# Kernel tuning notes

Measured on AMD Instinct MI355X. Metric: run time of the kernel, lower is better.

## Reference

```python
import jax, jax.numpy as jnp
import numpy as np

N_NODES = 100000
N_EDGES = 3200000
N_GRAPHS = 64
NEG_SLOPE = 0.2


def mish(x):
    return x * jnp.tanh(jax.nn.softplus(x))


def gat_layer(x, src, dst, W, b, a_src, a_dst, heads, out_ch, n_nodes):
    # h: [N, H, C]
    h = (x @ W).reshape(n_nodes, heads, out_ch)
    alpha_s = jnp.sum(h * a_src[None], axis=-1)  # [N, H]
    alpha_d = jnp.sum(h * a_dst[None], axis=-1)  # [N, H]
    e = jax.nn.leaky_relu(alpha_s[src] + alpha_d[dst], NEG_SLOPE)  # [E, H]
    # scatter-softmax over incoming edges of each destination node
    emax = jax.ops.segment_max(e, dst, num_segments=n_nodes)  # [N, H]
    ee = jnp.exp(e - emax[dst])
    den = jax.ops.segment_sum(ee, dst, num_segments=n_nodes)
    alpha = ee / (den[dst] + 1e-16)  # [E, H]
    msg = h[src] * alpha[..., None]  # [E, H, C]
    out = jax.ops.segment_sum(msg, dst, num_segments=n_nodes)
    return out.reshape(n_nodes, heads * out_ch) + b


def setup_inputs() -> dict:
    key = jax.random.key(0)
    ks = jax.random.split(key, 10)
    x = jax.random.normal(ks[0], (N_NODES, 128), dtype=jnp.float32)
    edge_index = jax.random.randint(ks[1], (2, N_EDGES), 0, N_NODES, dtype=jnp.int64)
    batch = jnp.sort(jax.random.randint(ks[2], (N_NODES,), 0, N_GRAPHS, dtype=jnp.int64))
    s1 = 1.0 / np.sqrt(128.0)
    s2 = 1.0 / np.sqrt(16.0)
    return {
        "x": x,
        "edge_index": edge_index,
        "batch": batch,
        "W1": jax.random.normal(ks[3], (128, 16), dtype=jnp.float32) * s1,
        "b1": jnp.zeros((16,), dtype=jnp.float32),
        "a_src1": jax.random.normal(ks[4], (4, 4), dtype=jnp.float32) * 0.5,
        "a_dst1": jax.random.normal(ks[5], (4, 4), dtype=jnp.float32) * 0.5,
        "W2": jax.random.normal(ks[6], (16, 32), dtype=jnp.float32) * s2,
        "b2": jnp.zeros((32,), dtype=jnp.float32),
        "a_src2": jax.random.normal(ks[7], (1, 32), dtype=jnp.float32) * 0.5,
        "a_dst2": jax.random.normal(ks[8], (1, 32), dtype=jnp.float32) * 0.5,
    }


def reference(x, edge_index, batch, W1, b1, a_src1, a_dst1, W2, b2, a_src2, a_dst2):
    n = x.shape[0]
    # PyG GATConv default add_self_loops=True
    loop = jnp.arange(n, dtype=edge_index.dtype)
    src = jnp.concatenate([edge_index[0], loop])
    dst = jnp.concatenate([edge_index[1], loop])
    h = mish(gat_layer(x, src, dst, W1, b1, a_src1, a_dst1, heads=4, out_ch=4, n_nodes=n))
    h = mish(gat_layer(h, src, dst, W2, b2, a_src2, a_dst2, heads=1, out_ch=32, n_nodes=n))
    # global_mean_pool
    sums = jax.ops.segment_sum(h, batch, num_segments=N_GRAPHS)
    cnts = jax.ops.segment_sum(jnp.ones((n,), h.dtype), batch, num_segments=N_GRAPHS)
    return sums / jnp.maximum(cnts, 1.0)[:, None]
```

## Files before the change

kernel.cpp:

```cpp
#include <hip/hip_runtime.h>
#include <hip/hip_fp16.h>
#include <math.h>

#define NEG_SLOPE 0.2f
#define SB 256
#define NBMAX 1024
#define CAP 5120
#define CAPH 2816

typedef _Float16 half2v __attribute__((ext_vector_type(2)));
typedef _Float16 half4v __attribute__((ext_vector_type(4)));

__device__ __forceinline__ float mishf(float x) {
    if (x > 15.f) return x;
    float ex = __expf(x);
    float y = 1.f + ex;
    float y2 = y * y;
    return x * (y2 - 1.f) / (y2 + 1.f);
}

__device__ __forceinline__ float lw(float e) {
    return __expf(fmaxf(e, NEG_SLOPE * e));
}

__device__ __forceinline__ float hdot2a(half2v a, half2v b, float c) {
#if __has_builtin(__builtin_amdgcn_fdot2)
    return __builtin_amdgcn_fdot2(a, b, c, false);
#else
    return (float)a.x * (float)b.x + (float)a.y * (float)b.y + c;
#endif
}

__global__ void gemm1_kernel(const float* __restrict__ x, const float* __restrict__ W1,
                             const float* __restrict__ a_dst,
                             const float* __restrict__ W2, const float* __restrict__ as2,
                             const float* __restrict__ ad2,
                             _Float16* __restrict__ hpre1h, float* __restrict__ addst,
                             int* __restrict__ cursor, float* __restrict__ pool,
                             float* __restrict__ cnt, float* __restrict__ vs,
                             float* __restrict__ vd, int NB, int NG, int N) {
    __shared__ float Wlt[16 * 132];
    __shared__ float xs[16 * 132];
    int tid = threadIdx.x;
    if (blockIdx.x == 0) {
        for (int i = tid; i < NB; i += 256) cursor[i] = 0;
        for (int i = tid; i < NG * 32; i += 256) pool[i] = 0.f;
        for (int i = tid; i < NG; i += 256) cnt[i] = 0.f;
        if (tid < 16) {
            float ps = 0.f, pd = 0.f;
            #pragma unroll
            for (int c = 0; c < 32; c++) {
                float w = W2[tid * 32 + c];
                ps += w * as2[c];
                pd += w * ad2[c];
            }
            vs[tid] = ps; vd[tid] = pd;
        }
    }
    for (int i = tid; i < 2048; i += 256) Wlt[(i & 15) * 132 + (i >> 4)] = W1[i];
    int nodebase = blockIdx.x * 16;
    const float4* x4 = (const float4*)(x + (size_t)nodebase * 128);
    for (int i = tid; i < 512; i += 256) {
        float4 v = x4[i];
        int e = i * 4;
        int nl = e >> 7, k = e & 127;
        float* dp = &xs[nl * 132 + k];
        dp[0] = v.x; dp[1] = v.y; dp[2] = v.z; dp[3] = v.w;
    }
    __syncthreads();
    int nl = tid >> 4, ch = tid & 15;
    const float4* xr4 = (const float4*)&xs[nl * 132];
    const float4* wr4 = (const float4*)&Wlt[ch * 132];
    float acc = 0.f;
    #pragma unroll
    for (int k4 = 0; k4 < 32; k4++) {
        float4 xv = xr4[k4];
        float4 wv = wr4[k4];
        acc += xv.x * wv.x + xv.y * wv.y + xv.z * wv.z + xv.w * wv.w;
    }
    int node = nodebase + nl;
    if (node < N) {
        hpre1h[node * 16 + ch] = (_Float16)acc;
        float pd = acc * a_dst[ch];
        pd += __shfl_xor(pd, 1); pd += __shfl_xor(pd, 2);
        if ((ch & 3) == 0) addst[node * 4 + (ch >> 2)] = pd;
    }
}

__global__ __launch_bounds__(1024) void scatF_kernel(
        const int* __restrict__ src, const int* __restrict__ dst,
        int E, int Etot, int CH, int NB,
        int* __restrict__ cursor, int* __restrict__ pairs) {
    __shared__ int lcnt[NBMAX];
    __shared__ int lbase[NBMAX];
    int tid = threadIdx.x, blk = blockIdx.x;
    for (int b = tid; b < NB; b += 1024) lcnt[b] = 0;
    __syncthreads();
    int ibeg = blk * CH, iend = min((blk + 1) * CH, Etot);
    int cd[16];
    #pragma unroll
    for (int u = 0; u < 16; u++) {
        int i = ibeg + tid + (u << 10);
        int d = -1;
        if (i < iend) d = (i < E) ? dst[i] : (i - E);
        cd[u] = d;
        if (d >= 0) atomicAdd(&lcnt[d >> 7], 1);
    }
    for (int i = ibeg + (16 << 10) + tid; i < iend; i += 1024) {
        int d = (i < E) ? dst[i] : (i - E);
        atomicAdd(&lcnt[d >> 7], 1);
    }
    __syncthreads();
    for (int b = tid; b < NB; b += 1024) {
        int h = lcnt[b];
        lbase[b] = h ? atomicAdd(&cursor[b], h) : 0;
    }
    __syncthreads();
    for (int b = tid; b < NB; b += 1024) lcnt[b] = 0;
    __syncthreads();
    #pragma unroll
    for (int u = 0; u < 16; u++) {
        int i = ibeg + tid + (u << 10);
        int d = cd[u];
        if (d < 0) continue;
        int s = (i < E) ? src[i] : d;
        int b = d >> 7, dl = d & 127;
        int r = atomicAdd(&lcnt[b], 1);
        int pos = lbase[b] + r;
        pairs[(size_t)b * CAP + (pos < CAP ? pos : CAP - 1)] = s | (dl << 17);
    }
    for (int i = ibeg + (16 << 10) + tid; i < iend; i += 1024) {
        int d = (i < E) ? dst[i] : (i - E);
        int s = (i < E) ? src[i] : d;
        int b = d >> 7, dl = d & 127;
        int r = atomicAdd(&lcnt[b], 1);
        int pos = lbase[b] + r;
        pairs[(size_t)b * CAP + (pos < CAP ? pos : CAP - 1)] = s | (dl << 17);
    }
}

__global__ __launch_bounds__(256) void csragg1_kernel(
        const int* __restrict__ pairs, const int* __restrict__ btotal,
        int NB, int N,
        int* __restrict__ ssorted, int* __restrict__ rs, int* __restrict__ re,
        const float* __restrict__ a_src1, const float* __restrict__ addst,
        const _Float16* __restrict__ hpre1h, const float* __restrict__ b1,
        const float* __restrict__ vs, const float* __restrict__ vd,
        _Float16* __restrict__ hpost1h,
        float* __restrict__ as2n, float* __restrict__ ad2n) {
    __shared__ int deg[64];
    __shared__ int s[64];
    __shared__ int cur[64];
    __shared__ int hcnt;
    __shared__ __attribute__((aligned(16))) int lds_raw[CAPH];
    __shared__ __attribute__((aligned(16))) int lds_sorted[CAPH];
    int tid = threadIdx.x, bh = blockIdx.x;
    int B = bh >> 1, half = bh & 1;
    int nb0 = (B << 7) + (half << 6);
    int cnt_nodes = min(64, N - nb0);
    int bstart = B * CAP;
    int total = min(btotal[B], CAP);
    if (tid < 64) deg[tid] = 0;
    if (tid == 0) hcnt = 0;
    __syncthreads();
    for (int j = tid; j < total; j += 256) {
        int p = pairs[bstart + j];
        if (((p >> 23) & 1) == half) {
            int r = atomicAdd(&hcnt, 1);
            if (r < CAPH) lds_raw[r] = p;
            atomicAdd(&deg[(p >> 17) & 63], 1);
        }
    }
    __syncthreads();
    if (tid < 64) s[tid] = deg[tid];
    __syncthreads();
    for (int o = 1; o < 64; o <<= 1) {
        int v = 0;
        if (tid < 64 && tid >= o) v = s[tid - o];
        __syncthreads();
        if (tid < 64) s[tid] += v;
        __syncthreads();
    }
    if (tid < 64) {
        int ex = s[tid] - deg[tid];
        cur[tid] = ex;
        if (tid < cnt_nodes) {
            rs[nb0 + tid] = bh * CAPH + ex;
            re[nb0 + tid] = bh * CAPH + ex + deg[tid];
        }
    }
    __syncthreads();
    int htot = min(hcnt, CAPH);
    for (int j = tid; j < htot; j += 256) {
        int p = lds_raw[j];
        int pos = atomicAdd(&cur[(p >> 17) & 63], 1);
        lds_sorted[pos < CAPH ? pos : CAPH - 1] = p & 0x1FFFF;
    }
    __syncthreads();

    {
        int t4 = htot >> 2;
        const int4* ls4 = (const int4*)lds_sorted;
        int4* gs4 = (int4*)(ssorted + (size_t)bh * CAPH);
        for (int j = tid; j < t4; j += 256) gs4[j] = ls4[j];
        for (int j = (t4 << 2) + tid; j < htot; j += 256)
            ssorted[(size_t)bh * CAPH + j] = lds_sorted[j];
    }

    int wave = tid >> 6;
    int lane = tid & 63;
    int head = lane & 3, er = lane >> 2;
    int c0 = head * 4;
    half2v w01, w23;
    w01.x = (_Float16)a_src1[c0];     w01.y = (_Float16)a_src1[c0 + 1];
    w23.x = (_Float16)a_src1[c0 + 2]; w23.y = (_Float16)a_src1[c0 + 3];
    for (int r = 0; r < 16; r++) {
        int ln = (wave << 4) + r;
        if (ln >= cnt_nodes) break;
        int node = nb0 + ln;
        int end = cur[ln];
        int start = end - deg[ln];
        float adh = addst[node * 4 + head];
        float den = 0.f, a0 = 0.f, a1 = 0.f, a2 = 0.f, a3 = 0.f;
        int last = end - 1;
        int jb = start;
        for (; jb + 16 <= end; jb += 16) {
            int s0 = lds_sorted[jb + er];
            half4v h = *(const half4v*)(hpre1h + (size_t)s0 * 16 + c0);
            half2v hlo = __builtin_shufflevector(h, h, 0, 1);
            half2v hhi = __builtin_shufflevector(h, h, 2, 3);
            float p = hdot2a(hlo, w01, hdot2a(hhi, w23, 0.f));
            float w = lw(p + adh);
            den += w;
            a0 += (float)h.x * w; a1 += (float)h.y * w;
            a2 += (float)h.z * w; a3 += (float)h.w * w;
        }
        if (jb < end) {
            int j0 = jb + er;
            int k0 = (j0 <= last) ? j0 : last;
            int s0 = lds_sorted[k0];
            half4v h = *(const half4v*)(hpre1h + (size_t)s0 * 16 + c0);
            half2v hlo = __builtin_shufflevector(h, h, 0, 1);
            half2v hhi = __builtin_shufflevector(h, h, 2, 3);
            float p = hdot2a(hlo, w01, hdot2a(hhi, w23, 0.f));
            float w = (j0 <= last) ? lw(p + adh) : 0.f;
            den += w;
            a0 += (float)h.x * w; a1 += (float)h.y * w;
            a2 += (float)h.z * w; a3 += (float)h.w * w;
        }
        a0 += __shfl_xor(a0, 4);  a1 += __shfl_xor(a1, 4);  a2 += __shfl_xor(a2, 4);  a3 += __shfl_xor(a3, 4);  den += __shfl_xor(den, 4);
        a0 += __shfl_xor(a0, 8);  a1 += __shfl_xor(a1, 8);  a2 += __shfl_xor(a2, 8);  a3 += __shfl_xor(a3, 8);  den += __shfl_xor(den, 8);
        a0 += __shfl_xor(a0, 16); a1 += __shfl_xor(a1, 16); a2 += __shfl_xor(a2, 16); a3 += __shfl_xor(a3, 16); den += __shfl_xor(den, 16);
        a0 += __shfl_xor(a0, 32); a1 += __shfl_xor(a1, 32); a2 += __shfl_xor(a2, 32); a3 += __shfl_xor(a3, 32); den += __shfl_xor(den, 32);
        if (er == 0) {
            float inv = 1.f / (den + 1e-16f);
            float o0 = mishf(a0 * inv + b1[c0]);
            float o1 = mishf(a1 * inv + b1[c0 + 1]);
            float o2 = mishf(a2 * inv + b1[c0 + 2]);
            float o3 = mishf(a3 * inv + b1[c0 + 3]);
            half4v oh;
            oh.x = (_Float16)o0; oh.y = (_Float16)o1;
            oh.z = (_Float16)o2; oh.w = (_Float16)o3;
            *(half4v*)(hpost1h + (size_t)node * 16 + c0) = oh;
            float ps = o0 * vs[c0] + o1 * vs[c0 + 1] + o2 * vs[c0 + 2] + o3 * vs[c0 + 3];
            float pd = o0 * vd[c0] + o1 * vd[c0 + 1] + o2 * vd[c0 + 2] + o3 * vd[c0 + 3];
            ps += __shfl_xor(ps, 1); pd += __shfl_xor(pd, 1);
            ps += __shfl_xor(ps, 2); pd += __shfl_xor(pd, 2);
            if (head == 0) { as2n[node] = ps; ad2n[node] = pd; }
        }
    }
}

__global__ void agg2_kernel(const int* __restrict__ rs, const int* __restrict__ re,
                            const int* __restrict__ ssorted,
                            const float* __restrict__ as2n, const float* __restrict__ ad2n,
                            const _Float16* __restrict__ hpost1h,
                            float* __restrict__ agg16, float* __restrict__ denv, int N) {
    int wave = threadIdx.x >> 6;
    int lane = threadIdx.x & 63;
    int node = blockIdx.x * 4 + wave;
    if (node >= N) return;
    int start = rs[node], end = re[node];
    int q = lane & 3, er = lane >> 2;
    int c0 = q * 4;
    float adh = ad2n[node];
    const _Float16* hb = hpost1h + c0;
    float den = 0.f, a0 = 0.f, a1 = 0.f, a2 = 0.f, a3 = 0.f;
    int last = end - 1;
    int jb = start;
    for (; jb + 16 <= end; jb += 16) {
        int s0 = __builtin_nontemporal_load(ssorted + jb + er);
        float w = lw(as2n[s0] + adh);
        half4v h = *(const half4v*)(hb + (size_t)s0 * 16);
        den += w;
        a0 += (float)h.x * w; a1 += (float)h.y * w;
        a2 += (float)h.z * w; a3 += (float)h.w * w;
    }
    if (jb < end) {
        int j0 = jb + er;
        int k0 = (j0 <= last) ? j0 : last;
        int s0 = __builtin_nontemporal_load(ssorted + k0);
        float w = (j0 <= last) ? lw(as2n[s0] + adh) : 0.f;
        half4v h = *(const half4v*)(hb + (size_t)s0 * 16);
        den += w;
        a0 += (float)h.x * w; a1 += (float)h.y * w;
        a2 += (float)h.z * w; a3 += (float)h.w * w;
    }
    a0 += __shfl_xor(a0, 4);  a1 += __shfl_xor(a1, 4);  a2 += __shfl_xor(a2, 4);  a3 += __shfl_xor(a3, 4);  den += __shfl_xor(den, 4);
    a0 += __shfl_xor(a0, 8);  a1 += __shfl_xor(a1, 8);  a2 += __shfl_xor(a2, 8);  a3 += __shfl_xor(a3, 8);  den += __shfl_xor(den, 8);
    a0 += __shfl_xor(a0, 16); a1 += __shfl_xor(a1, 16); a2 += __shfl_xor(a2, 16); a3 += __shfl_xor(a3, 16); den += __shfl_xor(den, 16);
    a0 += __shfl_xor(a0, 32); a1 += __shfl_xor(a1, 32); a2 += __shfl_xor(a2, 32); a3 += __shfl_xor(a3, 32); den += __shfl_xor(den, 32);
    if (er == 0) {
        float4 o; o.x = a0; o.y = a1; o.z = a2; o.w = a3;
        *(float4*)(agg16 + (size_t)node * 16 + c0) = o;
        if (q == 0) denv[node] = den;
    }
}

__global__ void post2pool_kernel(const float* __restrict__ agg16, const float* __restrict__ denv,
                                 const float* __restrict__ W2, const float* __restrict__ b2,
                                 const int* __restrict__ batch,
                                 float* __restrict__ pool, float* __restrict__ cnt, int N) {
    __shared__ float Wl[16 * 32];
    int tid = threadIdx.x;
    for (int i = tid; i < 512; i += 256) Wl[i] = W2[i];
    __syncthreads();
    int r = tid >> 5, ch = tid & 31;
    float bc = b2[ch];
    int base = blockIdx.x * 512;
    int cur = -1;
    float sum = 0.f, c = 0.f;
    for (int it = 0; it < 64; it++) {
        int n = base + it * 8 + r;
        if (n >= N) break;
        int g = batch[n];
        if (g != cur) {
            if (cur >= 0) {
                atomicAdd(&pool[cur * 32 + ch], sum);
                if (ch == 0) atomicAdd(&cnt[cur], c);
            }
            cur = g; sum = 0.f; c = 0.f;
        }
        const float* ar = agg16 + (size_t)n * 16;
        float acc = 0.f;
        #pragma unroll
        for (int k = 0; k < 16; k++) acc += ar[k] * Wl[k * 32 + ch];
        float val = mishf(acc / (denv[n] + 1e-16f) + bc);
        sum += val;
        c += 1.f;
    }
    if (cur >= 0) {
        atomicAdd(&pool[cur * 32 + ch], sum);
        if (ch == 0) atomicAdd(&cnt[cur], c);
    }
}

__global__ void fin_kernel(const float* __restrict__ pool, const float* __restrict__ cnt,
                           float* __restrict__ out, int NG) {
    int i = blockIdx.x * blockDim.x + threadIdx.x;
    if (i >= NG * 32) return;
    out[i] = pool[i] / fmaxf(cnt[i >> 5], 1.0f);
}

extern "C" void kernel_launch(void* const* d_in, const int* in_sizes, int n_in,
                              void* d_out, int out_size, void* d_ws, size_t ws_size,
                              hipStream_t stream) {
    const float* x   = (const float*)d_in[0];
    const int* eidx  = (const int*)d_in[1];
    const int* batch = (const int*)d_in[2];
    const float* W1  = (const float*)d_in[3];
    const float* b1  = (const float*)d_in[4];
    const float* as1 = (const float*)d_in[5];
    const float* ad1 = (const float*)d_in[6];
    const float* W2  = (const float*)d_in[7];
    const float* b2  = (const float*)d_in[8];
    const float* as2 = (const float*)d_in[9];
    const float* ad2 = (const float*)d_in[10];
    float* out = (float*)d_out;

    int N = in_sizes[0] / 128;
    int E = in_sizes[1] / 2;
    int Etot = E + N;
    int NG = out_size / 32;
    const int* esrc = eidx;
    const int* edst = eidx + E;

    int NB = (N + 127) >> 7;
    int NBH = NB * 2;
    int CH = (Etot + SB - 1) / SB;

    char* p = (char*)d_ws;
    auto alloc = [&](size_t nbytes) {
        p = (char*)(((uintptr_t)p + 15) & ~(uintptr_t)15);
        void* r = (void*)p; p += nbytes; return r;
    };
    int* pairs        = (int*)alloc((size_t)NB * CAP * 4);
    int* ssorted      = (int*)alloc((size_t)NBH * CAPH * 4);
    int* rs           = (int*)alloc((size_t)N * 4);
    int* re           = (int*)alloc((size_t)N * 4);
    int* cursor       = (int*)alloc((size_t)NB * 4);
    _Float16* hpre1h  = (_Float16*)alloc((size_t)N * 16 * 2);
    _Float16* hpost1h = (_Float16*)alloc((size_t)N * 16 * 2);
    float* addst1  = (float*)alloc((size_t)N * 4 * 4);
    float* as2n    = (float*)alloc((size_t)N * 4);
    float* ad2n    = (float*)alloc((size_t)N * 4);
    float* agg16   = (float*)alloc((size_t)N * 16 * 4);
    float* denv    = (float*)alloc((size_t)N * 4);
    float* vs      = (float*)alloc(16 * 4);
    float* vd      = (float*)alloc(16 * 4);
    float* pool    = (float*)alloc((size_t)NG * 32 * 4);
    float* cnt     = (float*)alloc((size_t)NG * 4);

    gemm1_kernel<<<(N + 15) / 16, 256, 0, stream>>>(x, W1, ad1, W2, as2, ad2,
                                                    hpre1h, addst1, cursor, pool, cnt,
                                                    vs, vd, NB, NG, N);
    scatF_kernel<<<SB, 1024, 0, stream>>>(esrc, edst, E, Etot, CH, NB, cursor, pairs);
    csragg1_kernel<<<NBH, 256, 0, stream>>>(pairs, cursor, NB, N,
                                            ssorted, rs, re, as1, addst1, hpre1h,
                                            b1, vs, vd, hpost1h, as2n, ad2n);
    agg2_kernel<<<(N + 3) / 4, 256, 0, stream>>>(rs, re, ssorted, as2n, ad2n, hpost1h,
                                                 agg16, denv, N);
    post2pool_kernel<<<(N + 511) / 512, 256, 0, stream>>>(agg16, denv, W2, b2, batch,
                                                          pool, cnt, N);
    fin_kernel<<<(NG * 32 + 255) / 256, 256, 0, stream>>>(pool, cnt, out, NG);
}
```

Before: 351.4 us.

## Fuse GEMM1 and edge scatter into one kernel with half-bucket binning

Merges the first-layer node GEMM and the edge bucketing scatter into a single launch, where some blocks run a grid-strided GEMM and the rest bin edges. Edges are now binned directly into 64-node half-buckets, with the two halves written from opposite ends of each bucket region. This lets the CSR kernel read its half directly instead of filtering the whole bucket through LDS. Counter zeroing moves to memsets and the pooling kernel uses smaller per-block chunks. The fused kernel needs a large LDS allocation at 1024 threads, and each half-bucket now has a tighter capacity limit.

```diff
diff --git a/kernel.cpp b/kernel.cpp
--- a/kernel.cpp
+++ b/kernel.cpp
@@ -3,10 +3,11 @@
 #include <math.h>
 
 #define NEG_SLOPE 0.2f
+#define GB 192
 #define SB 256
 #define NBMAX 1024
 #define CAP 5120
-#define CAPH 2816
+#define CAPH 2560
 
 typedef _Float16 half2v __attribute__((ext_vector_type(2)));
 typedef _Float16 half4v __attribute__((ext_vector_type(4)));
@@ -31,22 +32,22 @@
 #endif
 }
 
-__global__ void gemm1_kernel(const float* __restrict__ x, const float* __restrict__ W1,
-                             const float* __restrict__ a_dst,
-                             const float* __restrict__ W2, const float* __restrict__ as2,
-                             const float* __restrict__ ad2,
-                             _Float16* __restrict__ hpre1h, float* __restrict__ addst,
-                             int* __restrict__ cursor, float* __restrict__ pool,
-                             float* __restrict__ cnt, float* __restrict__ vs,
-                             float* __restrict__ vd, int NB, int NG, int N) {
-    __shared__ float Wlt[16 * 132];
-    __shared__ float xs[16 * 132];
+__global__ __launch_bounds__(1024) void front_kernel(
+        const float* __restrict__ x, const float* __restrict__ W1,
+        const float* __restrict__ a_dst,
+        const float* __restrict__ W2, const float* __restrict__ as2,
+        const float* __restrict__ ad2,
+        _Float16* __restrict__ hpre1h, float* __restrict__ addst,
+        float* __restrict__ vs, float* __restrict__ vd,
+        const int* __restrict__ src, const int* __restrict__ dst,
+        int E, int Etot, int CH, int NB, int N, int NT,
+        int* __restrict__ cursor, int* __restrict__ pairs) {
+    __shared__ __attribute__((aligned(16))) char smem[42240];
     int tid = threadIdx.x;
-    if (blockIdx.x == 0) {
-        for (int i = tid; i < NB; i += 256) cursor[i] = 0;
-        for (int i = tid; i < NG * 32; i += 256) pool[i] = 0.f;
-        for (int i = tid; i < NG; i += 256) cnt[i] = 0.f;
-        if (tid < 16) {
+    if (blockIdx.x < GB) {
+        float* Wlt = (float*)smem;
+        float* xs  = Wlt + 16 * 132;
+        if (blockIdx.x == 0 && tid < 16) {
             float ps = 0.f, pd = 0.f;
             #pragma unroll
             for (int c = 0; c < 32; c++) {
@@ -56,86 +57,94 @@
             }
             vs[tid] = ps; vd[tid] = pd;
         }
-    }
-    for (int i = tid; i < 2048; i += 256) Wlt[(i & 15) * 132 + (i >> 4)] = W1[i];
-    int nodebase = blockIdx.x * 16;
-    const float4* x4 = (const float4*)(x + (size_t)nodebase * 128);
-    for (int i = tid; i < 512; i += 256) {
-        float4 v = x4[i];
-        int e = i * 4;
-        int nl = e >> 7, k = e & 127;
-        float* dp = &xs[nl * 132 + k];
-        dp[0] = v.x; dp[1] = v.y; dp[2] = v.z; dp[3] = v.w;
-    }
-    __syncthreads();
-    int nl = tid >> 4, ch = tid & 15;
-    const float4* xr4 = (const float4*)&xs[nl * 132];
-    const float4* wr4 = (const float4*)&Wlt[ch * 132];
-    float acc = 0.f;
-    #pragma unroll
-    for (int k4 = 0; k4 < 32; k4++) {
-        float4 xv = xr4[k4];
-        float4 wv = wr4[k4];
-        acc += xv.x * wv.x + xv.y * wv.y + xv.z * wv.z + xv.w * wv.w;
-    }
-    int node = nodebase + nl;
-    if (node < N) {
-        hpre1h[node * 16 + ch] = (_Float16)acc;
-        float pd = acc * a_dst[ch];
-        pd += __shfl_xor(pd, 1); pd += __shfl_xor(pd, 2);
-        if ((ch & 3) == 0) addst[node * 4 + (ch >> 2)] = pd;
-    }
-}
-
-__global__ __launch_bounds__(1024) void scatF_kernel(
-        const int* __restrict__ src, const int* __restrict__ dst,
-        int E, int Etot, int CH, int NB,
-        int* __restrict__ cursor, int* __restrict__ pairs) {
-    __shared__ int lcnt[NBMAX];
-    __shared__ int lbase[NBMAX];
-    int tid = threadIdx.x, blk = blockIdx.x;
-    for (int b = tid; b < NB; b += 1024) lcnt[b] = 0;
-    __syncthreads();
-    int ibeg = blk * CH, iend = min((blk + 1) * CH, Etot);
-    int cd[16];
-    #pragma unroll
-    for (int u = 0; u < 16; u++) {
-        int i = ibeg + tid + (u << 10);
-        int d = -1;
-        if (i < iend) d = (i < E) ? dst[i] : (i - E);
-        cd[u] = d;
-        if (d >= 0) atomicAdd(&lcnt[d >> 7], 1);
-    }
-    for (int i = ibeg + (16 << 10) + tid; i < iend; i += 1024) {
-        int d = (i < E) ? dst[i] : (i - E);
-        atomicAdd(&lcnt[d >> 7], 1);
-    }
-    __syncthreads();
-    for (int b = tid; b < NB; b += 1024) {
-        int h = lcnt[b];
-        lbase[b] = h ? atomicAdd(&cursor[b], h) : 0;
-    }
-    __syncthreads();
-    for (int b = tid; b < NB; b += 1024) lcnt[b] = 0;
-    __syncthreads();
-    #pragma unroll
-    for (int u = 0; u < 16; u++) {
-        int i = ibeg + tid + (u << 10);
-        int d = cd[u];
-        if (d < 0) continue;
-        int s = (i < E) ? src[i] : d;
-        int b = d >> 7, dl = d & 127;
-        int r = atomicAdd(&lcnt[b], 1);
-        int pos = lbase[b] + r;
-        pairs[(size_t)b * CAP + (pos < CAP ? pos : CAP - 1)] = s | (dl << 17);
-    }
-    for (int i = ibeg + (16 << 10) + tid; i < iend; i += 1024) {
-        int d = (i < E) ? dst[i] : (i - E);
-        int s = (i < E) ? src[i] : d;
-        int b = d >> 7, dl = d & 127;
-        int r = atomicAdd(&lcnt[b], 1);
-        int pos = lbase[b] + r;
-        pairs[(size_t)b * CAP + (pos < CAP ? pos : CAP - 1)] = s | (dl << 17);
+        for (int i = tid; i < 2048; i += 1024) Wlt[(i & 15) * 132 + (i >> 4)] = W1[i];
+        int nl = tid >> 4, ch = tid & 15;
+        for (int t = blockIdx.x; t < NT; t += GB) {
+            int nodebase = t * 64;
+            int nvalid = min(64, N - nodebase);
+            __syncthreads();
+            const float4* x4 = (const float4*)(x + (size_t)nodebase * 128);
+            #pragma unroll
+            for (int u = 0; u < 2; u++) {
+                int i = tid + (u << 10);
+                int tnl = i >> 5;
+                if (tnl < nvalid) {
+                    float4 v = x4[i];
+                    int k = (i & 31) * 4;
+                    float* dp = &xs[tnl * 132 + k];
+                    dp[0] = v.x; dp[1] = v.y; dp[2] = v.z; dp[3] = v.w;
+                }
+            }
+            __syncthreads();
+            if (nl < nvalid) {
+                const float4* xr4 = (const float4*)&xs[nl * 132];
+                const float4* wr4 = (const float4*)&Wlt[ch * 132];
+                float acc = 0.f;
+                #pragma unroll
+                for (int k4 = 0; k4 < 32; k4++) {
+                    float4 xv = xr4[k4];
+                    float4 wv = wr4[k4];
+                    acc += xv.x * wv.x + xv.y * wv.y + xv.z * wv.z + xv.w * wv.w;
+                }
+                int node = nodebase + nl;
+                hpre1h[node * 16 + ch] = (_Float16)acc;
+                float pd = acc * a_dst[ch];
+                pd += __shfl_xor(pd, 1); pd += __shfl_xor(pd, 2);
+                if ((ch & 3) == 0) addst[node * 4 + (ch >> 2)] = pd;
+            }
+        }
+    } else {
+        int* lcnt  = (int*)smem;
+        int* lbase = lcnt + 2 * NBMAX;
+        int blk = blockIdx.x - GB;
+        int nb2 = 2 * NB;
+        for (int b = tid; b < nb2; b += 1024) lcnt[b] = 0;
+        __syncthreads();
+        int ibeg = blk * CH, iend = min((blk + 1) * CH, Etot);
+        int cd[16];
+        #pragma unroll
+        for (int u = 0; u < 16; u++) {
+            int i = ibeg + tid + (u << 10);
+            int d = -1;
+            if (i < iend) d = (i < E) ? dst[i] : (i - E);
+            cd[u] = d;
+            if (d >= 0) atomicAdd(&lcnt[d >> 6], 1);
+        }
+        for (int i = ibeg + (16 << 10) + tid; i < iend; i += 1024) {
+            int d = (i < E) ? dst[i] : (i - E);
+            atomicAdd(&lcnt[d >> 6], 1);
+        }
+        __syncthreads();
+        for (int b = tid; b < nb2; b += 1024) {
+            int h = lcnt[b];
+            lbase[b] = h ? atomicAdd(&cursor[b], h) : 0;
+        }
+        __syncthreads();
+        for (int b = tid; b < nb2; b += 1024) lcnt[b] = 0;
+        __syncthreads();
+        #pragma unroll
+        for (int u = 0; u < 16; u++) {
+            int i = ibeg + tid + (u << 10);
+            int d = cd[u];
+            if (d < 0) continue;
+            int s = (i < E) ? src[i] : d;
+            int idx2 = d >> 6;
+            int r = atomicAdd(&lcnt[idx2], 1);
+            int pos = lbase[idx2] + r;
+            pos = pos < CAPH ? pos : CAPH - 1;
+            size_t addr = (size_t)(idx2 >> 1) * CAP + ((idx2 & 1) ? (CAP - 1 - pos) : pos);
+            pairs[addr] = s | ((d & 63) << 17);
+        }
+        for (int i = ibeg + (16 << 10) + tid; i < iend; i += 1024) {
+            int d = (i < E) ? dst[i] : (i - E);
+            int s = (i < E) ? src[i] : d;
+            int idx2 = d >> 6;
+            int r = atomicAdd(&lcnt[idx2], 1);
+            int pos = lbase[idx2] + r;
+            pos = pos < CAPH ? pos : CAPH - 1;
+            size_t addr = (size_t)(idx2 >> 1) * CAP + ((idx2 & 1) ? (CAP - 1 - pos) : pos);
+            pairs[addr] = s | ((d & 63) << 17);
+        }
     }
 }
 
@@ -151,26 +160,17 @@
     __shared__ int deg[64];
     __shared__ int s[64];
     __shared__ int cur[64];
-    __shared__ int hcnt;
-    __shared__ __attribute__((aligned(16))) int lds_raw[CAPH];
     __shared__ __attribute__((aligned(16))) int lds_sorted[CAPH];
     int tid = threadIdx.x, bh = blockIdx.x;
     int B = bh >> 1, half = bh & 1;
     int nb0 = (B << 7) + (half << 6);
     int cnt_nodes = min(64, N - nb0);
-    int bstart = B * CAP;
-    int total = min(btotal[B], CAP);
+    int c = min(btotal[bh], CAPH);
+    int rbase = B * CAP + (half ? CAP - c : 0);
     if (tid < 64) deg[tid] = 0;
-    if (tid == 0) hcnt = 0;
-    __syncthreads();
-    for (int j = tid; j < total; j += 256) {
-        int p = pairs[bstart + j];
-        if (((p >> 23) & 1) == half) {
-            int r = atomicAdd(&hcnt, 1);
-            if (r < CAPH) lds_raw[r] = p;
-            atomicAdd(&deg[(p >> 17) & 63], 1);
-        }
-    }
+    __syncthreads();
+    for (int j = tid; j < c; j += 256)
+        atomicAdd(&deg[(pairs[rbase + j] >> 17) & 63], 1);
     __syncthreads();
     if (tid < 64) s[tid] = deg[tid];
     __syncthreads();
@@ -190,20 +190,19 @@
         }
     }
     __syncthreads();
-    int htot = min(hcnt, CAPH);
-    for (int j = tid; j < htot; j += 256) {
-        int p = lds_raw[j];
+    for (int j = tid; j < c; j += 256) {
+        int p = pairs[rbase + j];
         int pos = atomicAdd(&cur[(p >> 17) & 63], 1);
         lds_sorted[pos < CAPH ? pos : CAPH - 1] = p & 0x1FFFF;
     }
     __syncthreads();
 
     {
-        int t4 = htot >> 2;
+        int t4 = c >> 2;
         const int4* ls4 = (const int4*)lds_sorted;
         int4* gs4 = (int4*)(ssorted + (size_t)bh * CAPH);
         for (int j = tid; j < t4; j += 256) gs4[j] = ls4[j];
-        for (int j = (t4 << 2) + tid; j < htot; j += 256)
+        for (int j = (t4 << 2) + tid; j < c; j += 256)
             ssorted[(size_t)bh * CAPH + j] = lds_sorted[j];
     }
 
@@ -327,10 +326,10 @@
     __syncthreads();
     int r = tid >> 5, ch = tid & 31;
     float bc = b2[ch];
-    int base = blockIdx.x * 512;
+    int base = blockIdx.x * 128;
     int cur = -1;
     float sum = 0.f, c = 0.f;
-    for (int it = 0; it < 64; it++) {
+    for (int it = 0; it < 16; it++) {
         int n = base + it * 8 + r;
         if (n >= N) break;
         int g = batch[n];
@@ -387,6 +386,7 @@
 
     int NB = (N + 127) >> 7;
     int NBH = NB * 2;
+    int NT = (N + 63) >> 6;
     int CH = (Etot + SB - 1) / SB;
 
     char* p = (char*)d_ws;
@@ -398,7 +398,7 @@
     int* ssorted      = (int*)alloc((size_t)NBH * CAPH * 4);
     int* rs           = (int*)alloc((size_t)N * 4);
     int* re           = (int*)alloc((size_t)N * 4);
-    int* cursor       = (int*)alloc((size_t)NB * 4);
+    int* cursor       = (int*)alloc((size_t)NBH * 4);
     _Float16* hpre1h  = (_Float16*)alloc((size_t)N * 16 * 2);
     _Float16* hpost1h = (_Float16*)alloc((size_t)N * 16 * 2);
     float* addst1  = (float*)alloc((size_t)N * 4 * 4);
@@ -411,16 +411,20 @@
     float* pool    = (float*)alloc((size_t)NG * 32 * 4);
     float* cnt     = (float*)alloc((size_t)NG * 4);
 
-    gemm1_kernel<<<(N + 15) / 16, 256, 0, stream>>>(x, W1, ad1, W2, as2, ad2,
-                                                    hpre1h, addst1, cursor, pool, cnt,
-                                                    vs, vd, NB, NG, N);
-    scatF_kernel<<<SB, 1024, 0, stream>>>(esrc, edst, E, Etot, CH, NB, cursor, pairs);
+    hipMemsetAsync(cursor, 0, (size_t)NBH * 4, stream);
+    hipMemsetAsync(pool, 0, (size_t)NG * 32 * 4, stream);
+    hipMemsetAsync(cnt, 0, (size_t)NG * 4, stream);
+
+    front_kernel<<<GB + SB, 1024, 0, stream>>>(x, W1, ad1, W2, as2, ad2,
+                                               hpre1h, addst1, vs, vd,
+                                               esrc, edst, E, Etot, CH, NB, N, NT,
+                                               cursor, pairs);
     csragg1_kernel<<<NBH, 256, 0, stream>>>(pairs, cursor, NB, N,
                                             ssorted, rs, re, as1, addst1, hpre1h,
                                             b1, vs, vd, hpost1h, as2n, ad2n);
     agg2_kernel<<<(N + 3) / 4, 256, 0, stream>>>(rs, re, ssorted, as2n, ad2n, hpost1h,
                                                  agg16, denv, N);
-    post2pool_kernel<<<(N + 511) / 512, 256, 0, stream>>>(agg16, denv, W2, b2, batch,
+    post2pool_kernel<<<(N + 127) / 128, 256, 0, stream>>>(agg16, denv, W2, b2, batch,
                                                           pool, cnt, N);
     fin_kernel<<<(NG * 32 + 255) / 256, 256, 0, stream>>>(pool, cnt, out, NG);
 }
```

Result: faster. 330.4 us (-6.0%).
